# Kernel tuning notes

Measured on AMD Instinct MI355X. Metric: run time of the kernel, lower is better.

The kernel has to match this reference:

```python
import jax, jax.numpy as jnp
import numpy as np

NUM_HEADS = 12
HEAD_DIM = 64  # hidden 768 / 12


def setup_inputs() -> dict:
    key = jax.random.key(0)
    k1, k2, k3, k4 = jax.random.split(key, 4)
    B, S, H = 8, 1024, 768
    scale = 1.0 / np.sqrt(H)
    hidden_states = jax.random.normal(k1, (B, S, H), dtype=jnp.float32)
    Wq = jax.random.normal(k2, (H, H), dtype=jnp.float32) * scale
    Wk = jax.random.normal(k3, (H, H), dtype=jnp.float32) * scale
    Wv = jax.random.normal(k4, (H, H), dtype=jnp.float32) * scale
    return {"hidden_states": hidden_states, "Wq": Wq, "Wk": Wk, "Wv": Wv}


def reference(hidden_states, Wq, Wk, Wv):
    B, S, H = hidden_states.shape
    nh, hd = NUM_HEADS, HEAD_DIM
    # Linear projections, no bias. torch Linear: x @ W.T with W of shape [out, in];
    # here weights are stored [out, in] == [H, H].
    def proj(W):
        y = jnp.einsum('bsh,oh->bso', hidden_states, W)
        return y.reshape(B, S, nh, hd).transpose(0, 2, 1, 3)  # [B, nh, S, hd]
    q = proj(Wq)
    k = proj(Wk)
    v = proj(Wv)
    scale = 1.0 / np.sqrt(hd).astype(np.float32)
    scores = jnp.einsum('bhqd,bhkd->bhqk', q, k) * scale  # [B, nh, S, S]
    probs = jax.nn.softmax(scores, axis=-1)
    ctx = jnp.einsum('bhqk,bhkd->bhqd', probs, v)  # [B, nh, S, hd]
    ctx = ctx.transpose(0, 2, 1, 3).reshape(B, S, nh * hd)  # [B, S, H]
    return ctx
```

## Files before the change

### kernel.cpp

```cpp
#include <hip/hip_runtime.h>
#include <hip/hip_fp16.h>

typedef _Float16 f16;
typedef _Float16 f16x4 __attribute__((ext_vector_type(4)));
typedef _Float16 f16x8 __attribute__((ext_vector_type(8)));
typedef float f32x4 __attribute__((ext_vector_type(4)));

#define GLB_AS __attribute__((address_space(1)))
#define LDS_AS __attribute__((address_space(3)))

__device__ __forceinline__ void gload_lds16(const f16* g, f16* lds) {
    __builtin_amdgcn_global_load_lds((const GLB_AS uint32_t*)g,
                                     (LDS_AS uint32_t*)lds, 16, 0, 0);
}

__device__ __forceinline__ int swz(int r, int c8) {
    return r * 64 + (((c8) ^ (r & 7)) << 3);
}

__global__ void cvt_all(const float* __restrict__ hs, const float* __restrict__ wq,
                        const float* __restrict__ wk, const float* __restrict__ wv,
                        f16* __restrict__ hs16, f16* __restrict__ w16) {
    int i = blockIdx.x * 256 + threadIdx.x;
    const float4* src;
    f16x4* dst;
    int off;
    if (i < 1572864) {
        src = (const float4*)hs; dst = (f16x4*)hs16; off = i;
    } else {
        int j = i - 1572864;
        int w = j / 147456;
        off = j - w * 147456;
        src = (const float4*)(w == 0 ? wq : (w == 1 ? wk : wv));
        dst = (f16x4*)(w16 + (size_t)w * 589824);
    }
    float4 v = src[off];
    f16x4 h = {(f16)v.x, (f16)v.y, (f16)v.z, (f16)v.w};
    dst[off] = h;
}

#define QSCALE 0.18033688011112043f

__global__ __launch_bounds__(256, 3) void qkv_gemm(
        const f16* __restrict__ A, const f16* __restrict__ W,
        f16* __restrict__ Qh, f16* __restrict__ Kh, f16* __restrict__ Vth) {
    __shared__ f16 As[128 * 64];
    __shared__ f16 Bs[128 * 64];
    const int m0 = blockIdx.x * 128;
    const int n0 = blockIdx.y * 128;
    const int tid = threadIdx.x;
    const int wave = tid >> 6, lane = tid & 63;
    const int wm = wave & 1, wn = wave >> 1;
    const int quad = lane >> 4, l16 = lane & 15;
    const int srow = lane >> 3;
    const int scol = (((lane & 7) ^ srow) << 3);

    f32x4 acc[4][4] = {};

    const f16* Abase = A + (size_t)m0 * 768;
    const f16* Wbase = W + (size_t)n0 * 768;

    for (int kt = 0; kt < 12; ++kt) {
        const int k0 = kt * 64;
        __syncthreads();
#pragma unroll
        for (int j = 0; j < 4; ++j) {
            int inst = wave * 4 + j;
            int row = inst * 8 + srow;
            gload_lds16(Abase + (size_t)row * 768 + k0 + scol, &As[inst * 512]);
            gload_lds16(Wbase + (size_t)row * 768 + k0 + scol, &Bs[inst * 512]);
        }
        __syncthreads();
#pragma unroll
        for (int kk = 0; kk < 2; ++kk) {
            f16x8 af[4], bf[4];
#pragma unroll
            for (int mi = 0; mi < 4; ++mi) {
                int r = wm * 64 + mi * 16 + l16;
                af[mi] = *(const f16x8*)&As[swz(r, kk * 4 + quad)];
            }
#pragma unroll
            for (int ni = 0; ni < 4; ++ni) {
                int r = wn * 64 + ni * 16 + l16;
                bf[ni] = *(const f16x8*)&Bs[swz(r, kk * 4 + quad)];
            }
#pragma unroll
            for (int mi = 0; mi < 4; ++mi)
#pragma unroll
                for (int ni = 0; ni < 4; ++ni)
                    acc[mi][ni] = __builtin_amdgcn_mfma_f32_16x16x32_f16(
                        af[mi], bf[ni], acc[mi][ni], 0, 0, 0);
        }
    }

    const int seg = n0 / 768;
    const int obase = n0 - seg * 768;
    const float scale = (seg == 0) ? QSCALE : 1.0f;
#pragma unroll
    for (int mi = 0; mi < 4; ++mi) {
#pragma unroll
        for (int ni = 0; ni < 4; ++ni) {
            int o = obase + wn * 64 + ni * 16 + l16;
            int h = o >> 6, d = o & 63;
#pragma unroll
            for (int r = 0; r < 4; ++r) {
                int gm = m0 + wm * 64 + mi * 16 + quad * 4 + r;
                int b = gm >> 10, s = gm & 1023;
                size_t bh = (size_t)(b * 12 + h);
                f16 val = (f16)(acc[mi][ni][r] * scale);
                if (seg == 0)
                    Qh[((bh << 10 | s) << 6) + d] = val;
                else if (seg == 1)
                    Kh[((bh << 10 | s) << 6) + d] = val;
                else
                    Vth[(bh << 16) + ((size_t)d << 10) + s] = val;
            }
        }
    }
}

__global__ __launch_bounds__(256, 3) void attn(
        const f16* __restrict__ Qh, const f16* __restrict__ Kh,
        const f16* __restrict__ Vth, float* __restrict__ out) {
    __shared__ f16 Qs[64 * 64];
    __shared__ f16 Ks[2][64 * 64];
    __shared__ f16 Vts[2][64 * 64];
    __shared__ f16 Ps[4][16 * 72];
    const int bh = blockIdx.x;
    const int q0 = blockIdx.y * 64;
    const int b = bh / 12, h = bh % 12;
    const int tid = threadIdx.x, wave = tid >> 6, lane = tid & 63;
    const int quad = lane >> 4, l16 = lane & 15;
    const int srow = lane >> 3;
    const int scol = (((lane & 7) ^ srow) << 3);

    const f16* qbase = Qh + ((size_t)bh * 1024 + q0) * 64;
    const f16* kbase = Kh + (size_t)bh * 1024 * 64;
    const f16* vtbase = Vth + (size_t)bh * 64 * 1024;

#pragma unroll
    for (int j = 0; j < 2; ++j) {
        int inst = wave * 2 + j;
        int row = inst * 8 + srow;
        gload_lds16(qbase + row * 64 + scol, &Qs[inst * 512]);
    }
#pragma unroll
    for (int j = 0; j < 2; ++j) {
        int inst = wave * 2 + j;
        int row = inst * 8 + srow;
        gload_lds16(kbase + (size_t)row * 64 + scol, &Ks[0][inst * 512]);
        gload_lds16(vtbase + (size_t)row * 1024 + scol, &Vts[0][inst * 512]);
    }
    __syncthreads();

    f16x8 qa[2];
    qa[0] = *(const f16x8*)&Qs[swz(wave * 16 + l16, quad)];
    qa[1] = *(const f16x8*)&Qs[swz(wave * 16 + l16, 4 + quad)];

    f32x4 o_acc[4] = {};
    float rsum[4] = {0.f, 0.f, 0.f, 0.f};

    for (int kb = 0; kb < 16; ++kb) {
        const int cur = kb & 1;
        if (kb < 15) {
            const int nk0 = (kb + 1) * 64;
#pragma unroll
            for (int j = 0; j < 2; ++j) {
                int inst = wave * 2 + j;
                int row = inst * 8 + srow;
                gload_lds16(kbase + (size_t)(nk0 + row) * 64 + scol,
                            &Ks[cur ^ 1][inst * 512]);
                gload_lds16(vtbase + (size_t)row * 1024 + nk0 + scol,
                            &Vts[cur ^ 1][inst * 512]);
            }
        }

        f32x4 s_acc[4] = {};
#pragma unroll
        for (int ct = 0; ct < 4; ++ct) {
            f16x8 kb0 = *(const f16x8*)&Ks[cur][swz(ct * 16 + l16, quad)];
            f16x8 kb1 = *(const f16x8*)&Ks[cur][swz(ct * 16 + l16, 4 + quad)];
            s_acc[ct] = __builtin_amdgcn_mfma_f32_16x16x32_f16(qa[0], kb0, s_acc[ct], 0, 0, 0);
            s_acc[ct] = __builtin_amdgcn_mfma_f32_16x16x32_f16(qa[1], kb1, s_acc[ct], 0, 0, 0);
        }

#pragma unroll
        for (int ct = 0; ct < 4; ++ct)
#pragma unroll
            for (int r = 0; r < 4; ++r) {
                float p = __builtin_amdgcn_exp2f(s_acc[ct][r]);
                rsum[r] += p;
                Ps[wave][(quad * 4 + r) * 72 + ct * 16 + l16] = (f16)p;
            }
        f16x8 pa[2];
        pa[0] = *(const f16x8*)&Ps[wave][l16 * 72 + quad * 8];
        pa[1] = *(const f16x8*)&Ps[wave][l16 * 72 + 32 + quad * 8];

#pragma unroll
        for (int ct = 0; ct < 4; ++ct) {
            f16x8 vb0 = *(const f16x8*)&Vts[cur][swz(ct * 16 + l16, quad)];
            f16x8 vb1 = *(const f16x8*)&Vts[cur][swz(ct * 16 + l16, 4 + quad)];
            o_acc[ct] = __builtin_amdgcn_mfma_f32_16x16x32_f16(pa[0], vb0, o_acc[ct], 0, 0, 0);
            o_acc[ct] = __builtin_amdgcn_mfma_f32_16x16x32_f16(pa[1], vb1, o_acc[ct], 0, 0, 0);
        }

        if (kb < 15) __syncthreads();
    }

    float rinv[4];
#pragma unroll
    for (int r = 0; r < 4; ++r) {
        float rs = rsum[r];
#pragma unroll
        for (int off = 1; off <= 8; off <<= 1)
            rs += __shfl_xor(rs, off, 64);
        rinv[r] = 1.0f / rs;
    }

#pragma unroll
    for (int ct = 0; ct < 4; ++ct)
#pragma unroll
        for (int r = 0; r < 4; ++r) {
            int s = q0 + wave * 16 + quad * 4 + r;
            int d = ct * 16 + l16;
            out[((size_t)b * 1024 + s) * 768 + (size_t)h * 64 + d] =
                o_acc[ct][r] * rinv[r];
        }
}

extern "C" void kernel_launch(void* const* d_in, const int* in_sizes, int n_in,
                              void* d_out, int out_size, void* d_ws, size_t ws_size,
                              hipStream_t stream) {
    const float* hs = (const float*)d_in[0];
    const float* Wq = (const float*)d_in[1];
    const float* Wk = (const float*)d_in[2];
    const float* Wv = (const float*)d_in[3];
    float* out = (float*)d_out;

    char* ws = (char*)d_ws;
    f16* hs16 = (f16*)ws;
    f16* w16  = (f16*)(ws + 12582912);
    f16* Qh   = (f16*)(ws + 16121856);
    f16* Kh   = (f16*)(ws + 28704768);
    f16* Vth  = (f16*)(ws + 41287680);

    cvt_all<<<7872, 256, 0, stream>>>(hs, Wq, Wk, Wv, hs16, w16);
    qkv_gemm<<<dim3(64, 18), 256, 0, stream>>>(hs16, w16, Qh, Kh, Vth);
    attn<<<dim3(96, 16), 256, 0, stream>>>(Qh, Kh, Vth, out);
    (void)in_sizes; (void)n_in; (void)out_size; (void)ws_size;
}
```

Baseline: 184.0 us.

## Double query tile per attention block, compute S transposed, vectorize V^T stores

The attention kernel now processes 128 queries per block, with each wave handling two 16-row tiles. This reuses each K/V tile loaded into LDS across twice as many queries and halves the grid. Scores are computed as K·Q^T so each lane holds four consecutive keys, which lets P be written to LDS as packed f16x4 with an XOR swizzle. P reuses the Q staging buffer after the Q fragments are loaded into registers. Separately, the QKV GEMM epilogue writes V^T as 4-wide vector stores instead of scalar ones. The trade-off is higher register pressure (two sets of accumulators) and fewer blocks available for occupancy.

```diff
diff --git a/kernel.cpp b/kernel.cpp
--- a/kernel.cpp
+++ b/kernel.cpp
@@ -2,6 +2,7 @@
 #include <hip/hip_fp16.h>
 
 typedef _Float16 f16;
+typedef _Float16 f16x2 __attribute__((ext_vector_type(2)));
 typedef _Float16 f16x4 __attribute__((ext_vector_type(4)));
 typedef _Float16 f16x8 __attribute__((ext_vector_type(8)));
 typedef float f32x4 __attribute__((ext_vector_type(4)));
@@ -102,18 +103,22 @@
         for (int ni = 0; ni < 4; ++ni) {
             int o = obase + wn * 64 + ni * 16 + l16;
             int h = o >> 6, d = o & 63;
-#pragma unroll
-            for (int r = 0; r < 4; ++r) {
-                int gm = m0 + wm * 64 + mi * 16 + quad * 4 + r;
-                int b = gm >> 10, s = gm & 1023;
+            if (seg == 2) {
+                int gm0 = m0 + wm * 64 + mi * 16 + quad * 4;
+                int b = gm0 >> 10, s = gm0 & 1023;
                 size_t bh = (size_t)(b * 12 + h);
-                f16 val = (f16)(acc[mi][ni][r] * scale);
-                if (seg == 0)
-                    Qh[((bh << 10 | s) << 6) + d] = val;
-                else if (seg == 1)
-                    Kh[((bh << 10 | s) << 6) + d] = val;
-                else
-                    Vth[(bh << 16) + ((size_t)d << 10) + s] = val;
+                f16x4 v4 = {(f16)acc[mi][ni][0], (f16)acc[mi][ni][1],
+                            (f16)acc[mi][ni][2], (f16)acc[mi][ni][3]};
+                *(f16x4*)&Vth[(bh << 16) + ((size_t)d << 10) + s] = v4;
+            } else {
+                f16* dst = (seg == 0) ? Qh : Kh;
+#pragma unroll
+                for (int r = 0; r < 4; ++r) {
+                    int gm = m0 + wm * 64 + mi * 16 + quad * 4 + r;
+                    int b = gm >> 10, s = gm & 1023;
+                    size_t bh = (size_t)(b * 12 + h);
+                    dst[((bh << 10 | s) << 6) + d] = (f16)(acc[mi][ni][r] * scale);
+                }
             }
         }
     }
@@ -122,12 +127,11 @@
 __global__ __launch_bounds__(256, 3) void attn(
         const f16* __restrict__ Qh, const f16* __restrict__ Kh,
         const f16* __restrict__ Vth, float* __restrict__ out) {
-    __shared__ f16 Qs[64 * 64];
+    __shared__ f16 QsPt[128 * 64];
     __shared__ f16 Ks[2][64 * 64];
     __shared__ f16 Vts[2][64 * 64];
-    __shared__ f16 Ps[4][16 * 72];
     const int bh = blockIdx.x;
-    const int q0 = blockIdx.y * 64;
+    const int q0 = blockIdx.y * 128;
     const int b = bh / 12, h = bh % 12;
     const int tid = threadIdx.x, wave = tid >> 6, lane = tid & 63;
     const int quad = lane >> 4, l16 = lane & 15;
@@ -139,10 +143,10 @@
     const f16* vtbase = Vth + (size_t)bh * 64 * 1024;
 
 #pragma unroll
-    for (int j = 0; j < 2; ++j) {
-        int inst = wave * 2 + j;
+    for (int j = 0; j < 4; ++j) {
+        int inst = wave * 4 + j;
         int row = inst * 8 + srow;
-        gload_lds16(qbase + row * 64 + scol, &Qs[inst * 512]);
+        gload_lds16(qbase + row * 64 + scol, &QsPt[inst * 512]);
     }
 #pragma unroll
     for (int j = 0; j < 2; ++j) {
@@ -153,12 +157,20 @@
     }
     __syncthreads();
 
-    f16x8 qa[2];
-    qa[0] = *(const f16x8*)&Qs[swz(wave * 16 + l16, quad)];
-    qa[1] = *(const f16x8*)&Qs[swz(wave * 16 + l16, 4 + quad)];
-
-    f32x4 o_acc[4] = {};
-    float rsum[4] = {0.f, 0.f, 0.f, 0.f};
+    f16x8 qa[2][2];
+#pragma unroll
+    for (int t = 0; t < 2; ++t)
+#pragma unroll
+        for (int kk = 0; kk < 2; ++kk)
+            qa[t][kk] = *(const f16x8*)&QsPt[swz(wave * 32 + t * 16 + l16, kk * 4 + quad)];
+    __syncthreads();
+
+    const int ptb0 = (wave * 2 + 0) * 1024;
+    const int ptb1 = (wave * 2 + 1) * 1024;
+    const int rowoff = l16 * 64;
+
+    f32x4 o_acc[2][4] = {};
+    float rsum[2] = {0.f, 0.f};
 
     for (int kb = 0; kb < 16; ++kb) {
         const int cur = kb & 1;
@@ -175,57 +187,78 @@
             }
         }
 
-        f32x4 s_acc[4] = {};
-#pragma unroll
-        for (int ct = 0; ct < 4; ++ct) {
-            f16x8 kb0 = *(const f16x8*)&Ks[cur][swz(ct * 16 + l16, quad)];
-            f16x8 kb1 = *(const f16x8*)&Ks[cur][swz(ct * 16 + l16, 4 + quad)];
-            s_acc[ct] = __builtin_amdgcn_mfma_f32_16x16x32_f16(qa[0], kb0, s_acc[ct], 0, 0, 0);
-            s_acc[ct] = __builtin_amdgcn_mfma_f32_16x16x32_f16(qa[1], kb1, s_acc[ct], 0, 0, 0);
-        }
-
+        f32x4 st[2][4] = {};
+#pragma unroll
+        for (int kk = 0; kk < 2; ++kk) {
+            f16x8 kf[4];
+#pragma unroll
+            for (int ct = 0; ct < 4; ++ct)
+                kf[ct] = *(const f16x8*)&Ks[cur][swz(ct * 16 + l16, kk * 4 + quad)];
+#pragma unroll
+            for (int t = 0; t < 2; ++t)
+#pragma unroll
+                for (int ct = 0; ct < 4; ++ct)
+                    st[t][ct] = __builtin_amdgcn_mfma_f32_16x16x32_f16(
+                        kf[ct], qa[t][kk], st[t][ct], 0, 0, 0);
+        }
+
+#pragma unroll
+        for (int t = 0; t < 2; ++t) {
+            const int ptb = t ? ptb1 : ptb0;
+#pragma unroll
+            for (int ct = 0; ct < 4; ++ct) {
+                float e0 = __builtin_amdgcn_exp2f(st[t][ct][0]);
+                float e1 = __builtin_amdgcn_exp2f(st[t][ct][1]);
+                float e2 = __builtin_amdgcn_exp2f(st[t][ct][2]);
+                float e3 = __builtin_amdgcn_exp2f(st[t][ct][3]);
+                rsum[t] += (e0 + e1) + (e2 + e3);
+                f16x4 pv = {(f16)e0, (f16)e1, (f16)e2, (f16)e3};
+                *(f16x4*)&QsPt[ptb + rowoff + (((ct * 4 + quad) ^ l16) << 2)] = pv;
+            }
+        }
+
+#pragma unroll
+        for (int kk = 0; kk < 2; ++kk) {
+            f16x8 vf[4];
+#pragma unroll
+            for (int ct = 0; ct < 4; ++ct)
+                vf[ct] = *(const f16x8*)&Vts[cur][swz(ct * 16 + l16, kk * 4 + quad)];
+#pragma unroll
+            for (int t = 0; t < 2; ++t) {
+                const int ptb = t ? ptb1 : ptb0;
+                int s8 = kk * 8 + quad * 2;
+                f16x4 plo = *(const f16x4*)&QsPt[ptb + rowoff + ((s8 ^ l16) << 2)];
+                f16x4 phi = *(const f16x4*)&QsPt[ptb + rowoff + (((s8 + 1) ^ l16) << 2)];
+                f16x8 pa = {plo.x, plo.y, plo.z, plo.w, phi.x, phi.y, phi.z, phi.w};
+#pragma unroll
+                for (int ct = 0; ct < 4; ++ct)
+                    o_acc[t][ct] = __builtin_amdgcn_mfma_f32_16x16x32_f16(
+                        pa, vf[ct], o_acc[t][ct], 0, 0, 0);
+            }
+        }
+
+        if (kb < 15) __syncthreads();
+    }
+
+#pragma unroll
+    for (int t = 0; t < 2; ++t) {
+        float rt = rsum[t];
+        rt += __shfl_xor(rt, 16, 64);
+        rt += __shfl_xor(rt, 32, 64);
+        float rv[4];
+#pragma unroll
+        for (int r = 0; r < 4; ++r)
+            rv[r] = 1.0f / __shfl(rt, quad * 4 + r, 64);
 #pragma unroll
         for (int ct = 0; ct < 4; ++ct)
 #pragma unroll
             for (int r = 0; r < 4; ++r) {
-                float p = __builtin_amdgcn_exp2f(s_acc[ct][r]);
-                rsum[r] += p;
-                Ps[wave][(quad * 4 + r) * 72 + ct * 16 + l16] = (f16)p;
-            }
-        f16x8 pa[2];
-        pa[0] = *(const f16x8*)&Ps[wave][l16 * 72 + quad * 8];
-        pa[1] = *(const f16x8*)&Ps[wave][l16 * 72 + 32 + quad * 8];
-
-#pragma unroll
-        for (int ct = 0; ct < 4; ++ct) {
-            f16x8 vb0 = *(const f16x8*)&Vts[cur][swz(ct * 16 + l16, quad)];
-            f16x8 vb1 = *(const f16x8*)&Vts[cur][swz(ct * 16 + l16, 4 + quad)];
-            o_acc[ct] = __builtin_amdgcn_mfma_f32_16x16x32_f16(pa[0], vb0, o_acc[ct], 0, 0, 0);
-            o_acc[ct] = __builtin_amdgcn_mfma_f32_16x16x32_f16(pa[1], vb1, o_acc[ct], 0, 0, 0);
-        }
-
-        if (kb < 15) __syncthreads();
-    }
-
-    float rinv[4];
-#pragma unroll
-    for (int r = 0; r < 4; ++r) {
-        float rs = rsum[r];
-#pragma unroll
-        for (int off = 1; off <= 8; off <<= 1)
-            rs += __shfl_xor(rs, off, 64);
-        rinv[r] = 1.0f / rs;
-    }
-
-#pragma unroll
-    for (int ct = 0; ct < 4; ++ct)
-#pragma unroll
-        for (int r = 0; r < 4; ++r) {
-            int s = q0 + wave * 16 + quad * 4 + r;
-            int d = ct * 16 + l16;
-            out[((size_t)b * 1024 + s) * 768 + (size_t)h * 64 + d] =
-                o_acc[ct][r] * rinv[r];
-        }
+                int s = q0 + wave * 32 + t * 16 + quad * 4 + r;
+                int d = ct * 16 + l16;
+                out[((size_t)b * 1024 + s) * 768 + (size_t)h * 64 + d] =
+                    o_acc[t][ct][r] * rv[r];
+            }
+    }
 }
 
 extern "C" void kernel_launch(void* const* d_in, const int* in_sizes, int n_in,
@@ -246,6 +279,6 @@
 
     cvt_all<<<7872, 256, 0, stream>>>(hs, Wq, Wk, Wv, hs16, w16);
     qkv_gemm<<<dim3(64, 18), 256, 0, stream>>>(hs16, w16, Qh, Kh, Vth);
-    attn<<<dim3(96, 16), 256, 0, stream>>>(Qh, Kh, Vth, out);
+    attn<<<dim3(96, 8), 256, 0, stream>>>(Qh, Kh, Vth, out);
     (void)in_sizes; (void)n_in; (void)out_size; (void)ws_size;
 }
```

Measured after the change: 160.6 us. 1.15x faster.
